# Kernel optimization log

Measured on AMD Instinct MI355X. Metric: run time of the kernel, lower is better.

Reference implementation:

```python
import jax, jax.numpy as jnp
import numpy as np

N, E, F, H, EF, ED, L, NL, NH, OD = 2048, 65536, 128, 512, 16, 64, 5, 4, 8, 64
MAX_DEG = 64


def _ln(x, s, b):
    m = x.mean(-1, keepdims=True)
    v = x.var(-1, keepdims=True)
    return (x - m) * jax.lax.rsqrt(v + 1e-5) * s + b


def setup_inputs() -> dict:
    key = jax.random.key(0)
    ks = jax.random.split(key, 40)
    s = 0.02
    x = jax.random.normal(ks[0], (N, F), jnp.float32)
    edge_index = jax.random.randint(ks[1], (2, E), 0, N, jnp.int32)
    edge_attr = jax.random.normal(ks[2], (E, EF), jnp.float32)
    # variable-length shortest paths, padded with -1
    plen = jax.random.randint(ks[3], (N, N), 0, L + 1, jnp.int32)
    pos = jnp.arange(L, dtype=jnp.int32)
    valid = pos[None, None, :] < plen[:, :, None]
    node_paths = jnp.where(valid, jax.random.randint(ks[4], (N, N, L), 0, N, jnp.int32), -1)
    edge_paths = jnp.where(valid, jax.random.randint(ks[5], (N, N, L), 0, E, jnp.int32), -1)
    p = {
        'x': x, 'edge_index': edge_index, 'edge_attr': edge_attr,
        'node_paths': node_paths, 'edge_paths': edge_paths,
        'W_node': s * jax.random.normal(ks[6], (F, H)), 'b_node': jnp.zeros((H,)),
        'W_edge': s * jax.random.normal(ks[7], (EF, ED)), 'b_edge': jnp.zeros((ED,)),
        'z_in': s * jax.random.normal(ks[8], (MAX_DEG, H)),
        'z_out': s * jax.random.normal(ks[9], (MAX_DEG, H)),
        'b_spatial': s * jax.random.normal(ks[10], (L,)),
        'edge_vector': s * jax.random.normal(ks[11], (L, ED)),
        'ln1_s': jnp.ones((NL, H)), 'ln1_b': jnp.zeros((NL, H)),
        'Wq': s * jax.random.normal(ks[12], (NL, H, H)), 'bq': jnp.zeros((NL, H)),
        'Wk': s * jax.random.normal(ks[13], (NL, H, H)), 'bk': jnp.zeros((NL, H)),
        'Wv': s * jax.random.normal(ks[14], (NL, H, H)), 'bv': jnp.zeros((NL, H)),
        'Wo': s * jax.random.normal(ks[15], (NL, H, H)), 'bo': jnp.zeros((NL, H)),
        'ln2_s': jnp.ones((NL, H)), 'ln2_b': jnp.zeros((NL, H)),
        'W1': s * jax.random.normal(ks[16], (NL, H, H)), 'b1': jnp.zeros((NL, H)),
        'W2': s * jax.random.normal(ks[17], (NL, H, H)), 'b2': jnp.zeros((NL, H)),
        'W_out': s * jax.random.normal(ks[18], (H, OD)), 'b_out': jnp.zeros((OD,)),
    }
    return p


def reference(x, edge_index, edge_attr, node_paths, edge_paths,
              W_node, b_node, W_edge, b_edge, z_in, z_out, b_spatial, edge_vector,
              ln1_s, ln1_b, Wq, bq, Wk, bk, Wv, bv, Wo, bo,
              ln2_s, ln2_b, W1, b1, W2, b2, W_out, b_out):
    n = x.shape[0]
    dk = H // NH
    h = x @ W_node + b_node  # [N,H]
    # centrality encoding: in/out degree -> learned embeddings, clamped
    in_deg = jnp.clip(jnp.zeros((n,), jnp.int32).at[edge_index[1]].add(1), 0, MAX_DEG - 1)
    out_deg = jnp.clip(jnp.zeros((n,), jnp.int32).at[edge_index[0]].add(1), 0, MAX_DEG - 1)
    h = h + z_in[in_deg] + z_out[out_deg]
    # edge encoding: mean over path of <edge_vector[k], edge_emb[path_k]>
    e_emb = edge_attr @ W_edge + b_edge           # [E,ED]
    w = e_emb @ edge_vector.T                     # [E,L] per-position dot products
    valid_e = edge_paths >= 0
    gath = w[jnp.clip(edge_paths, 0), jnp.arange(L)[None, None, :]]  # [N,N,L]
    cnt = valid_e.sum(-1).astype(h.dtype)
    c = jnp.where(cnt > 0, (gath * valid_e).sum(-1) / jnp.maximum(cnt, 1.0), 0.0)  # [N,N]
    # spatial encoding: learned scalar per path length
    plen = (node_paths >= 0).sum(-1)
    b_sp = jnp.where(plen > 0, b_spatial[jnp.clip(plen - 1, 0, L - 1)], 0.0)  # [N,N]
    bias = b_sp + c
    scale = 1.0 / jnp.sqrt(jnp.asarray(dk, h.dtype))
    for l in range(NL):
        y = _ln(h, ln1_s[l], ln1_b[l])
        q = (y @ Wq[l] + bq[l]).reshape(n, NH, dk)
        k = (y @ Wk[l] + bk[l]).reshape(n, NH, dk)
        v = (y @ Wv[l] + bv[l]).reshape(n, NH, dk)
        scores = jnp.einsum('ihd,jhd->hij', q, k) * scale + bias[None]
        attn = jax.nn.softmax(scores, axis=-1)
        o = jnp.einsum('hij,jhd->ihd', attn, v).reshape(n, H)
        h = h + o @ Wo[l] + bo[l]
        y2 = _ln(h, ln2_s[l], ln2_b[l])
        h = h + jax.nn.gelu(y2 @ W1[l] + b1[l]) @ W2[l] + b2[l]
    return h @ W_out + b_out
```

## Files before the change

### kernel.cpp

```cpp
#include <hip/hip_runtime.h>
#include <hip/hip_bf16.h>
#include <math.h>

#define N_NODES 2048
#define NEDGE   65536
#define FDIM    128
#define HDIM    512
#define EFD     16
#define EDD     64
#define LPATH   5
#define NLAYER  4
#define NHEAD   8
#define DK      64
#define ODIM    64
#define MAXDEG  64
#define PTOT    4194304

typedef __bf16 bf16;
typedef bf16 bf16x8 __attribute__((ext_vector_type(8)));
typedef bf16 bf16x4 __attribute__((ext_vector_type(4)));
typedef float f32x4 __attribute__((ext_vector_type(4)));
typedef unsigned short u16;

__global__ __launch_bounds__(256) void k_edge_w(const float* __restrict__ ea, const float* __restrict__ We,
                                                const float* __restrict__ be, const float* __restrict__ ev,
                                                const int* __restrict__ ei, int* __restrict__ din,
                                                int* __restrict__ dout, bf16* __restrict__ wT) {
    __shared__ float sM[80];
    __shared__ float sc[8];
    int t = threadIdx.x;
    if (t < 80) {
        int i = t / 5, j = t % 5;
        float acc = 0.f;
        for (int k = 0; k < EDD; ++k) acc += We[i * EDD + k] * ev[j * EDD + k];
        sM[t] = acc;
    } else if (t >= 128 && t < 128 + LPATH) {
        int j = t - 128;
        float acc = 0.f;
        for (int k = 0; k < EDD; ++k) acc += be[k] * ev[j * EDD + k];
        sc[j] = acc;
    }
    int e = blockIdx.x * 256 + t;
    atomicAdd(&dout[ei[e]], 1);
    atomicAdd(&din[ei[NEDGE + e]], 1);
    __syncthreads();
    const float4* p = (const float4*)(ea + (size_t)e * EFD);
    float4 a0 = p[0], a1 = p[1], a2 = p[2], a3 = p[3];
    float a[16] = {a0.x, a0.y, a0.z, a0.w, a1.x, a1.y, a1.z, a1.w,
                   a2.x, a2.y, a2.z, a2.w, a3.x, a3.y, a3.z, a3.w};
    float out[LPATH];
#pragma unroll
    for (int j = 0; j < LPATH; ++j) out[j] = sc[j];
#pragma unroll
    for (int i = 0; i < 16; ++i)
#pragma unroll
        for (int j = 0; j < LPATH; ++j) out[j] += a[i] * sM[i * LPATH + j];
#pragma unroll
    for (int j = 0; j < LPATH; ++j) wT[(size_t)j * NEDGE + e] = (bf16)out[j];
}

__global__ __launch_bounds__(1024) void k_bias3(const int* __restrict__ ep, const bf16* __restrict__ wT,
                                                const float* __restrict__ bsp, bf16* __restrict__ bias) {
    __shared__ char lds[163840];
    int t = threadIdx.x;
    size_t basep = (size_t)blockIdx.x * 8192;
    int* ish = (int*)lds;
    const int4* src = (const int4*)(ep + basep * 5);
#pragma unroll
    for (int u = 0; u < 10; ++u) ((int4*)ish)[t + 1024 * u] = src[t + 1024 * u];
    __syncthreads();
    unsigned pa[8], pb[8], pc[8];
#pragma unroll
    for (int r = 0; r < 8; ++r) {
        int p5 = (r * 1024 + t) * 5;
        int e0 = ish[p5], e1 = ish[p5 + 1], e2 = ish[p5 + 2], e3 = ish[p5 + 3], e4 = ish[p5 + 4];
        unsigned mk = (unsigned)(e0 >= 0) | ((unsigned)(e1 >= 0) << 1) | ((unsigned)(e2 >= 0) << 2)
                    | ((unsigned)(e3 >= 0) << 3) | ((unsigned)(e4 >= 0) << 4);
        pa[r] = ((unsigned)e0 & 0xFFFFu) | ((unsigned)e1 << 16);
        pb[r] = ((unsigned)e2 & 0xFFFFu) | ((unsigned)e3 << 16);
        pc[r] = ((unsigned)e4 & 0xFFFFu) | (mk << 16);
    }
    bf16* wsl = (bf16*)lds;
    float csum[8] = {};
#pragma unroll
    for (int l = 0; l < LPATH; ++l) {
        __syncthreads();
#pragma unroll
        for (int u = 0; u < 4; ++u) {
            int o = u * 16384 + t * 16;
            *(bf16x8*)&wsl[o]     = *(const bf16x8*)&wT[(size_t)l * NEDGE + o];
            *(bf16x8*)&wsl[o + 8] = *(const bf16x8*)&wT[(size_t)l * NEDGE + o + 8];
        }
        __syncthreads();
#pragma unroll
        for (int r = 0; r < 8; ++r) {
            unsigned ix = (l == 0) ? (pa[r] & 0xFFFFu) : (l == 1) ? (pa[r] >> 16)
                        : (l == 2) ? (pb[r] & 0xFFFFu) : (l == 3) ? (pb[r] >> 16) : (pc[r] & 0xFFFFu);
            float v = (float)wsl[ix];
            csum[r] += ((pc[r] >> (16 + l)) & 1u) ? v : 0.f;
        }
    }
#pragma unroll
    for (int r = 0; r < 8; ++r) {
        int cnt = __popc((int)((pc[r] >> 16) & 0x1Fu));
        float b = cnt ? bsp[cnt - 1] + csum[r] / (float)cnt : 0.f;
        bias[basep + r * 1024 + t] = (bf16)b;
    }
}

__global__ __launch_bounds__(256) void k_ln(const float* __restrict__ h, const float* __restrict__ sc,
                                            const float* __restrict__ bi, bf16* __restrict__ y) {
    int i = blockIdx.x, t = threadIdx.x;
    float v0 = h[(size_t)i * HDIM + t];
    float v1 = h[(size_t)i * HDIM + 256 + t];
    float s = v0 + v1, q = v0 * v0 + v1 * v1;
#pragma unroll
    for (int m = 1; m < 64; m <<= 1) { s += __shfl_xor(s, m); q += __shfl_xor(q, m); }
    __shared__ float ssum[4], sq[4];
    int wv = t >> 6;
    if ((t & 63) == 0) { ssum[wv] = s; sq[wv] = q; }
    __syncthreads();
    float S = ssum[0] + ssum[1] + ssum[2] + ssum[3];
    float Q = sq[0] + sq[1] + sq[2] + sq[3];
    float mean = S * (1.f / HDIM);
    float var = Q * (1.f / HDIM) - mean * mean;
    float r = rsqrtf(var + 1e-5f);
    y[(size_t)i * HDIM + t] = (bf16)((v0 - mean) * r * sc[t] + bi[t]);
    y[(size_t)i * HDIM + 256 + t] = (bf16)((v1 - mean) * r * sc[256 + t] + bi[256 + t]);
}

__global__ __launch_bounds__(256) void k_wprep(const float* __restrict__ Wq, const float* __restrict__ Wk,
                                               const float* __restrict__ Wv, const float* __restrict__ Wo,
                                               const float* __restrict__ W1, const float* __restrict__ W2,
                                               const float* __restrict__ Wn, bf16* __restrict__ Wt,
                                               bf16* __restrict__ WnT) {
    __shared__ float Ls[64][68];
    int m = blockIdx.y;
    int q = blockIdx.x;
    int t = threadIdx.x;
    int rr = t >> 4, cc = t & 15;
    int nl = t >> 2, kc = t & 3;
    if (m < 24) {
        int lay = m / 6, type = m % 6;
        const float* src = type == 0 ? Wq : type == 1 ? Wk : type == 2 ? Wv : type == 3 ? Wo : type == 4 ? W1 : W2;
        src += (size_t)lay * (HDIM * HDIM);
        int tk = q >> 3, tn = q & 7;
#pragma unroll
        for (int u = 0; u < 4; ++u) {
            float4 v = *(const float4*)(src + (size_t)(tk * 64 + rr + 16 * u) * HDIM + tn * 64 + cc * 4);
            *(float4*)&Ls[rr + 16 * u][cc * 4] = v;
        }
        __syncthreads();
        bf16 tmp[16];
#pragma unroll
        for (int u = 0; u < 16; ++u) tmp[u] = (bf16)Ls[kc * 16 + u][nl];
        bf16* dst = Wt + (size_t)m * (HDIM * HDIM) + (size_t)(tn * 64 + nl) * HDIM + tk * 64 + kc * 16;
        *(bf16x8*)(dst) = *(bf16x8*)&tmp[0];
        *(bf16x8*)(dst + 8) = *(bf16x8*)&tmp[8];
    } else {
        if (q >= 16) return;
        int tk = q >> 3, tn = q & 7;
#pragma unroll
        for (int u = 0; u < 4; ++u) {
            float4 v = *(const float4*)(Wn + (size_t)(tk * 64 + rr + 16 * u) * HDIM + tn * 64 + cc * 4);
            *(float4*)&Ls[rr + 16 * u][cc * 4] = v;
        }
        __syncthreads();
        bf16 tmp[16];
#pragma unroll
        for (int u = 0; u < 16; ++u) tmp[u] = (bf16)Ls[kc * 16 + u][nl];
        bf16* dst = WnT + (size_t)(tn * 64 + nl) * FDIM + tk * 64 + kc * 16;
        *(bf16x8*)dst = *(bf16x8*)&tmp[0];
        *(bf16x8*)(dst + 8) = *(bf16x8*)&tmp[8];
    }
}

__global__ __launch_bounds__(256) void k_nmm(const float* __restrict__ x, const bf16* __restrict__ Bt,
                                             const float* __restrict__ bn, const float* __restrict__ zin,
                                             const float* __restrict__ zout, const int* __restrict__ din,
                                             const int* __restrict__ dout, float* __restrict__ h) {
    __shared__ bf16 Bs[8192];
    int t = threadIdx.x, w = t >> 6, l = t & 63, lr = l & 15, lg = l >> 4;
    int j0 = blockIdx.x * 64, i0 = blockIdx.y * 64;
    const bf16* Bp = Bt + (size_t)j0 * FDIM;
#pragma unroll
    for (int rnd = 0; rnd < 4; ++rnd) {
        int tt = rnd * 256 + t;
        int ks = tt >> 8, qq = (tt >> 6) & 3, mm = (tt >> 2) & 15, gg = tt & 3;
        *(bf16x8*)(Bs + tt * 8) = *(const bf16x8*)(Bp + (size_t)(qq * 16 + mm) * FDIM + ks * 32 + gg * 8);
    }
    __syncthreads();
    const float* ap = x + (size_t)(i0 + w * 16 + lr) * FDIM + 8 * lg;
    f32x4 acc[4] = {};
#pragma unroll
    for (int ks = 0; ks < 4; ++ks) {
        float4 f0 = *(const float4*)(ap + ks * 32);
        float4 f1 = *(const float4*)(ap + ks * 32 + 4);
        bf16x8 a;
        a[0] = (bf16)f0.x; a[1] = (bf16)f0.y; a[2] = (bf16)f0.z; a[3] = (bf16)f0.w;
        a[4] = (bf16)f1.x; a[5] = (bf16)f1.y; a[6] = (bf16)f1.z; a[7] = (bf16)f1.w;
        const bf16* bb = Bs + ks * 2048 + lr * 32 + lg * 8;
#pragma unroll
        for (int sub = 0; sub < 4; ++sub)
            acc[sub] = __builtin_amdgcn_mfma_f32_16x16x32_bf16(a, *(const bf16x8*)(bb + sub * 512), acc[sub], 0, 0, 0);
    }
#pragma unroll
    for (int r = 0; r < 4; ++r) {
        int i = i0 + w * 16 + lg * 4 + r;
        int di = min(din[i], MAXDEG - 1), dz = min(dout[i], MAXDEG - 1);
#pragma unroll
        for (int sub = 0; sub < 4; ++sub) {
            int j = j0 + sub * 16 + lr;
            h[(size_t)i * HDIM + j] = acc[sub][r] + bn[j] + zin[(size_t)di * HDIM + j] + zout[(size_t)dz * HDIM + j];
        }
    }
}

__global__ __launch_bounds__(256) void k_qkv(const bf16* __restrict__ A, const bf16* __restrict__ Wt_l,
                                             const float* __restrict__ bq, const float* __restrict__ bk,
                                             const float* __restrict__ bv, bf16* __restrict__ qf,
                                             bf16* __restrict__ kf, bf16* __restrict__ vf) {
    __shared__ bf16 Bs[16384];
    int t = threadIdx.x, w = t >> 6, l = t & 63, lr = l & 15, lg = l >> 4;
    int j0 = blockIdx.x * 32, i0 = blockIdx.y * 64;
    int type = j0 >> 9, n0 = j0 & 511;
    const bf16* Bp = Wt_l + (size_t)type * (HDIM * HDIM) + (size_t)n0 * HDIM;
#pragma unroll
    for (int rnd = 0; rnd < 8; ++rnd) {
        int tt = rnd * 256 + t;
        int ks = tt >> 7, qq = (tt >> 6) & 1, mm = (tt >> 2) & 15, gg = tt & 3;
        bf16x8 v = *(const bf16x8*)(Bp + (size_t)(qq * 16 + mm) * HDIM + ks * 32 + gg * 8);
        *(bf16x8*)(Bs + tt * 8) = v;
    }
    __syncthreads();
    const bf16* ap = A + (size_t)(i0 + w * 16 + lr) * HDIM + 8 * lg;
    const float* bvec = (type == 0 ? bq : type == 1 ? bk : bv);
    f32x4 acc[2] = {};
#pragma unroll 4
    for (int ks = 0; ks < 16; ++ks) {
        bf16x8 a  = *(const bf16x8*)(ap + ks * 32);
        const bf16* bb = Bs + ks * 1024 + lr * 32 + lg * 8;
        bf16x8 b0 = *(const bf16x8*)(bb);
        bf16x8 b1 = *(const bf16x8*)(bb + 512);
        acc[0] = __builtin_amdgcn_mfma_f32_16x16x32_bf16(a, b0, acc[0], 0, 0, 0);
        acc[1] = __builtin_amdgcn_mfma_f32_16x16x32_bf16(a, b1, acc[1], 0, 0, 0);
    }
    int h = n0 >> 6;
    if (type < 2) {
        bf16* dst = (type == 0 ? qf : kf);
        int hf = (n0 & 32) >> 5;
        float sc = (type == 0 ? 0.125f : 1.0f);
#pragma unroll
        for (int sub = 0; sub < 2; ++sub) {
#pragma unroll
            for (int r = 0; r < 4; ++r) {
                int i = i0 + w * 16 + lg * 4 + r;
                float v = (acc[sub][r] + bvec[n0 + sub * 16 + lr]) * sc;
                int lgp = sub * 2 + (lr >> 3);
                size_t off = (((size_t)(h * 128 + (i >> 4)) * 2 + hf) << 9) + lgp * 128 + (lg * 4 + r) * 8 + (lr & 7);
                dst[off] = (bf16)v;
            }
        }
    } else {
#pragma unroll
        for (int sub = 0; sub < 2; ++sub) {
#pragma unroll
            for (int r = 0; r < 4; ++r) {
                int node = i0 + w * 16 + lg * 4 + r;
                int dd = (n0 & 63) + sub * 16 + lr;
                float v = acc[sub][r] + bvec[n0 + sub * 16 + lr];
                size_t off = (((size_t)(h * 4 + (dd >> 4)) * 64 + (node >> 5)) << 9)
                           + ((node >> 3) & 3) * 128 + (dd & 15) * 8 + (node & 7);
                vf[off] = (bf16)v;
            }
        }
    }
}

#define FL_RES   1
#define FL_GELU  2
#define FL_OUTF  4

__device__ inline float gelu_f(float x) {
    float x3 = x * x * x;
    float u = 0.7978845608028654f * (x + 0.044715f * x3);
    return 0.5f * x * (1.f + tanhf(u));
}

__global__ __launch_bounds__(1024) void k_mm(const bf16* __restrict__ A, const bf16* __restrict__ Bt,
                                             const float* __restrict__ bvec, const float* __restrict__ res,
                                             float* __restrict__ outF, bf16* __restrict__ outB, int flags) {
    __shared__ bf16 Bs[32768];
    __shared__ float Osh[4][16][68];
    int t = threadIdx.x, w = t >> 6, l = t & 63, lr = l & 15, lg = l >> 4;
    int ti = w & 3, s = w >> 2;
    int j0 = blockIdx.x * 64, i0 = blockIdx.y * 64;
    const bf16* Bp = Bt + (size_t)j0 * HDIM;
#pragma unroll
    for (int rnd = 0; rnd < 4; ++rnd) {
        int tt = rnd * 1024 + t;
        int ks = tt >> 8, qq = (tt >> 6) & 3, mm = (tt >> 2) & 15, gg = tt & 3;
        bf16x8 v = *(const bf16x8*)(Bp + (size_t)(qq * 16 + mm) * HDIM + ks * 32 + gg * 8);
        *(bf16x8*)(Bs + tt * 8) = v;
    }
    __syncthreads();
    const bf16* ap = A + (size_t)(i0 + ti * 16 + lr) * HDIM + 8 * lg;
    f32x4 acc[4] = {};
#pragma unroll
    for (int kk = 0; kk < 4; ++kk) {
        int ks = s * 4 + kk;
        bf16x8 a = *(const bf16x8*)(ap + ks * 32);
        const bf16* bb = Bs + ks * 2048 + lr * 32 + lg * 8;
#pragma unroll
        for (int sub = 0; sub < 4; ++sub) {
            bf16x8 b = *(const bf16x8*)(bb + sub * 512);
            acc[sub] = __builtin_amdgcn_mfma_f32_16x16x32_bf16(a, b, acc[sub], 0, 0, 0);
        }
    }
    if (s == 0) {
#pragma unroll
        for (int sub = 0; sub < 4; ++sub)
#pragma unroll
            for (int r = 0; r < 4; ++r) Osh[ti][lg * 4 + r][sub * 16 + lr] = acc[sub][r];
    }
    __syncthreads();
    if (s == 1) {
#pragma unroll
        for (int sub = 0; sub < 4; ++sub)
#pragma unroll
            for (int r = 0; r < 4; ++r) Osh[ti][lg * 4 + r][sub * 16 + lr] += acc[sub][r];
    }
    __syncthreads();
    if (s == 2) {
#pragma unroll
        for (int sub = 0; sub < 4; ++sub)
#pragma unroll
            for (int r = 0; r < 4; ++r) Osh[ti][lg * 4 + r][sub * 16 + lr] += acc[sub][r];
    }
    __syncthreads();
    if (s == 3) {
#pragma unroll
        for (int sub = 0; sub < 4; ++sub) {
#pragma unroll
            for (int r = 0; r < 4; ++r) {
                int i = i0 + ti * 16 + lg * 4 + r;
                int j = j0 + sub * 16 + lr;
                float v = Osh[ti][lg * 4 + r][sub * 16 + lr] + acc[sub][r] + bvec[j];
                if (flags & FL_RES) v += res[(size_t)i * HDIM + j];
                if (flags & FL_GELU) v = gelu_f(v);
                if (flags & FL_OUTF) outF[(size_t)i * HDIM + j] = v;
                else outB[(size_t)i * HDIM + j] = (bf16)v;
            }
        }
    }
}

__global__ __launch_bounds__(1024) void k_mmln(const float* __restrict__ h, const bf16* __restrict__ Bt,
                                               const float* __restrict__ lnS, const float* __restrict__ lnB,
                                               const float* __restrict__ bvec, bf16* __restrict__ outB) {
    __shared__ bf16 As[32768];
    __shared__ bf16 Bs[32768];
    __shared__ float Osh[4][16][68];
    __shared__ float sbuf[HDIM], bbuf[HDIM];
    int t = threadIdx.x, w = t >> 6, l = t & 63, lr = l & 15, lg = l >> 4;
    int ti = w & 3, s = w >> 2;
    int j0 = blockIdx.x * 64, i0 = blockIdx.y * 64;
    if (t < HDIM) sbuf[t] = lnS[t];
    else bbuf[t - HDIM] = lnB[t - HDIM];
    const bf16* Bp = Bt + (size_t)j0 * HDIM;
#pragma unroll
    for (int rnd = 0; rnd < 4; ++rnd) {
        int tt = rnd * 1024 + t;
        int ks = tt >> 8, qq = (tt >> 6) & 3, mm = (tt >> 2) & 15, gg = tt & 3;
        *(bf16x8*)(Bs + tt * 8) = *(const bf16x8*)(Bp + (size_t)(qq * 16 + mm) * HDIM + ks * 32 + gg * 8);
    }
    int row = t >> 4, ksc = t & 15;
    const float* hp = h + (size_t)(i0 + row) * HDIM + ksc * 32;
    float4 hv[8];
    float S = 0.f, Q = 0.f;
#pragma unroll
    for (int u = 0; u < 8; ++u) {
        hv[u] = *(const float4*)(hp + u * 4);
        S += hv[u].x + hv[u].y + hv[u].z + hv[u].w;
        Q += hv[u].x * hv[u].x + hv[u].y * hv[u].y + hv[u].z * hv[u].z + hv[u].w * hv[u].w;
    }
#pragma unroll
    for (int m = 1; m < 16; m <<= 1) { S += __shfl_xor(S, m); Q += __shfl_xor(Q, m); }
    float mean = S * (1.f / HDIM);
    float var = Q * (1.f / HDIM) - mean * mean;
    float rr = rsqrtf(var + 1e-5f);
    float ca = rr, cc = -mean * rr;
    __syncthreads();
    {
        bf16 tmp[32];
#pragma unroll
        for (int u = 0; u < 8; ++u) {
            float vv[4] = {hv[u].x, hv[u].y, hv[u].z, hv[u].w};
#pragma unroll
            for (int c = 0; c < 4; ++c) {
                int col = ksc * 32 + u * 4 + c;
                tmp[u * 4 + c] = (bf16)(fmaf(fmaf(vv[c], ca, cc), sbuf[col], bbuf[col]));
            }
        }
        bf16* dst = As + (row >> 4) * 8192 + ksc * 512 + (row & 15) * 32;
#pragma unroll
        for (int u = 0; u < 4; ++u) *(bf16x8*)(dst + u * 8) = *(bf16x8*)&tmp[u * 8];
    }
    __syncthreads();
    const bf16* apl = As + ti * 8192 + lr * 32 + lg * 8;
    f32x4 acc[4] = {};
#pragma unroll
    for (int kk = 0; kk < 4; ++kk) {
        int ks = s * 4 + kk;
        bf16x8 a = *(const bf16x8*)(apl + ks * 512);
        const bf16* bb = Bs + ks * 2048 + lr * 32 + lg * 8;
#pragma unroll
        for (int sub = 0; sub < 4; ++sub)
            acc[sub] = __builtin_amdgcn_mfma_f32_16x16x32_bf16(a, *(const bf16x8*)(bb + sub * 512), acc[sub], 0, 0, 0);
    }
    if (s == 0) {
#pragma unroll
        for (int sub = 0; sub < 4; ++sub)
#pragma unroll
            for (int r = 0; r < 4; ++r) Osh[ti][lg * 4 + r][sub * 16 + lr] = acc[sub][r];
    }
    __syncthreads();
    if (s == 1) {
#pragma unroll
        for (int sub = 0; sub < 4; ++sub)
#pragma unroll
            for (int r = 0; r < 4; ++r) Osh[ti][lg * 4 + r][sub * 16 + lr] += acc[sub][r];
    }
    __syncthreads();
    if (s == 2) {
#pragma unroll
        for (int sub = 0; sub < 4; ++sub)
#pragma unroll
            for (int r = 0; r < 4; ++r) Osh[ti][lg * 4 + r][sub * 16 + lr] += acc[sub][r];
    }
    __syncthreads();
    if (s == 3) {
#pragma unroll
        for (int sub = 0; sub < 4; ++sub) {
#pragma unroll
            for (int r = 0; r < 4; ++r) {
                int i = i0 + ti * 16 + lg * 4 + r;
                int j = j0 + sub * 16 + lr;
                float v = gelu_f(Osh[ti][lg * 4 + r][sub * 16 + lr] + acc[sub][r] + bvec[j]);
                outB[(size_t)i * HDIM + j] = (bf16)v;
            }
        }
    }
}

__global__ __launch_bounds__(1024) void k_attn2(const bf16* __restrict__ qf, const bf16* __restrict__ kf,
                                                const bf16* __restrict__ vf, const bf16* __restrict__ biasb,
                                                bf16* __restrict__ ob) {
    __shared__ char Pb[16 * 1024];
    __shared__ float Osh[4][64][17];
    __shared__ float Msh[4][4][16], Lsh[4][4][16];
    int t = threadIdx.x, w = t >> 6, l = t & 63, lr = l & 15, lg = l >> 4;
    int ti = w & 3, s = w >> 2;
    int bid = blockIdx.x;
    int wid = (bid & 7) * 32 + (bid >> 3);
    int i0 = (wid >> 3) * 64, hh = wid & 7;
    int irow = i0 + ti * 16;

    const bf16* qb = qf + (((size_t)(hh * 128 + (irow >> 4)) * 2) << 9) + l * 8;
    bf16x8 qy0 = *(const bf16x8*)(qb);
    bf16x8 qy1 = *(const bf16x8*)(qb + 512);

    char* pwr = Pb + w * 1024 + lr * 64;
    unsigned kx = (unsigned)(lr & 6) << 3;

    float m_run = -3e38f, l_run = 0.f;
    f32x4 oacc[4] = {};

    int jb0 = s * 512;
    const bf16* kbp = kf + (((size_t)(hh * 128 + (jb0 >> 4)) * 2) << 9) + l * 8;
    bf16x8 ka0 = *(const bf16x8*)(kbp);
    bf16x8 ka1 = *(const bf16x8*)(kbp + 512);
    bf16x8 ka2 = *(const bf16x8*)(kbp + 1024);
    bf16x8 ka3 = *(const bf16x8*)(kbp + 1536);
    const bf16* bpp = biasb + (size_t)(irow + lr) * N_NODES + jb0 + lg * 4;
    bf16x4 ba0 = *(const bf16x4*)(bpp);
    bf16x4 ba1 = *(const bf16x4*)(bpp + 16);

    for (int it = 0; it < 16; ++it) {
        int jb = s * 512 + it * 32;
        const bf16* vb = vf + (((size_t)(hh * 4) * 64 + (jb >> 5)) << 9) + l * 8;
        bf16x8 vx0 = *(const bf16x8*)(vb);
        bf16x8 vx1 = *(const bf16x8*)(vb + 32768);
        bf16x8 vx2 = *(const bf16x8*)(vb + 65536);
        bf16x8 vx3 = *(const bf16x8*)(vb + 98304);
        bf16x8 kn0, kn1, kn2, kn3;
        bf16x4 bn0, bn1;
        if (it < 15) {
            int jn = jb + 32;
            const bf16* kbn = kf + (((size_t)(hh * 128 + (jn >> 4)) * 2) << 9) + l * 8;
            kn0 = *(const bf16x8*)(kbn);
            kn1 = *(const bf16x8*)(kbn + 512);
            kn2 = *(const bf16x8*)(kbn + 1024);
            kn3 = *(const bf16x8*)(kbn + 1536);
            const bf16* bpn = biasb + (size_t)(irow + lr) * N_NODES + jn + lg * 4;
            bn0 = *(const bf16x4*)(bpn);
            bn1 = *(const bf16x4*)(bpn + 16);
        }

        f32x4 s0v = {}, s1v = {};
        __builtin_amdgcn_s_setprio(1);
        s0v = __builtin_amdgcn_mfma_f32_16x16x32_bf16(ka0, qy0, s0v, 0, 0, 0);
        s0v = __builtin_amdgcn_mfma_f32_16x16x32_bf16(ka1, qy1, s0v, 0, 0, 0);
        s1v = __builtin_amdgcn_mfma_f32_16x16x32_bf16(ka2, qy0, s1v, 0, 0, 0);
        s1v = __builtin_amdgcn_mfma_f32_16x16x32_bf16(ka3, qy1, s1v, 0, 0, 0);
        __builtin_amdgcn_s_setprio(0);

        float p0[4], p1[4];
        float mt = -3e38f;
#pragma unroll
        for (int r = 0; r < 4; ++r) {
            p0[r] = s0v[r] + (float)ba0[r];
            p1[r] = s1v[r] + (float)ba1[r];
            mt = fmaxf(mt, fmaxf(p0[r], p1[r]));
        }
        mt = fmaxf(mt, __shfl_xor(mt, 16));
        mt = fmaxf(mt, __shfl_xor(mt, 32));
        if (!__all(mt <= m_run + 8.f)) {
            float mn = fmaxf(m_run, mt);
            float alpha = __expf(m_run - mn);
            l_run *= alpha;
#pragma unroll
            for (int d = 0; d < 4; ++d) oacc[d] *= alpha;
            m_run = mn;
        }
        float ps = 0.f;
        bf16x4 pk0, pk1;
#pragma unroll
        for (int r = 0; r < 4; ++r) {
            p0[r] = __expf(p0[r] - m_run);
            p1[r] = __expf(p1[r] - m_run);
            ps += p0[r] + p1[r];
            pk0[r] = (bf16)p0[r];
            pk1[r] = (bf16)p1[r];
        }
        ps += __shfl_xor(ps, 16);
        ps += __shfl_xor(ps, 32);
        l_run += ps;

        *(bf16x4*)(pwr + ((lg * 8) ^ kx)) = pk0;
        *(bf16x4*)(pwr + ((32 + lg * 8) ^ kx)) = pk1;
        asm volatile("s_waitcnt lgkmcnt(0)" ::: "memory");
        __builtin_amdgcn_sched_barrier(0x20);
        bf16x8 py = *(bf16x8*)(Pb + w * 1024 + lr * 64 + ((lg * 16) ^ kx));
        __builtin_amdgcn_s_setprio(1);
        oacc[0] = __builtin_amdgcn_mfma_f32_16x16x32_bf16(vx0, py, oacc[0], 0, 0, 0);
        oacc[1] = __builtin_amdgcn_mfma_f32_16x16x32_bf16(vx1, py, oacc[1], 0, 0, 0);
        oacc[2] = __builtin_amdgcn_mfma_f32_16x16x32_bf16(vx2, py, oacc[2], 0, 0, 0);
        oacc[3] = __builtin_amdgcn_mfma_f32_16x16x32_bf16(vx3, py, oacc[3], 0, 0, 0);
        __builtin_amdgcn_s_setprio(0);
        ka0 = kn0; ka1 = kn1; ka2 = kn2; ka3 = kn3;
        ba0 = bn0; ba1 = bn1;
    }

    __syncthreads();
    if (lg == 0) { Msh[ti][s][lr] = m_run; Lsh[ti][s][lr] = l_run; }
    __syncthreads();
    float m0 = Msh[ti][0][lr], m1 = Msh[ti][1][lr], m2 = Msh[ti][2][lr], m3 = Msh[ti][3][lr];
    float mtot = fmaxf(fmaxf(m0, m1), fmaxf(m2, m3));
    float l_tot = Lsh[ti][0][lr] * __expf(m0 - mtot) + Lsh[ti][1][lr] * __expf(m1 - mtot)
                + Lsh[ti][2][lr] * __expf(m2 - mtot) + Lsh[ti][3][lr] * __expf(m3 - mtot);
    float fac = __expf(m_run - mtot);
#pragma unroll
    for (int d = 0; d < 4; ++d) oacc[d] *= fac;
    if (s == 0) {
#pragma unroll
        for (int db = 0; db < 4; ++db)
#pragma unroll
            for (int r = 0; r < 4; ++r) Osh[ti][db * 16 + lg * 4 + r][lr] = oacc[db][r];
    }
    __syncthreads();
    if (s == 1) {
#pragma unroll
        for (int db = 0; db < 4; ++db)
#pragma unroll
            for (int r = 0; r < 4; ++r) Osh[ti][db * 16 + lg * 4 + r][lr] += oacc[db][r];
    }
    __syncthreads();
    if (s == 2) {
#pragma unroll
        for (int db = 0; db < 4; ++db)
#pragma unroll
            for (int r = 0; r < 4; ++r) Osh[ti][db * 16 + lg * 4 + r][lr] += oacc[db][r];
    }
    __syncthreads();
    if (s == 3) {
        float inv = 1.f / l_tot;
#pragma unroll
        for (int db = 0; db < 4; ++db) {
            bf16x4 o4;
#pragma unroll
            for (int r = 0; r < 4; ++r)
                o4[r] = (bf16)((Osh[ti][db * 16 + lg * 4 + r][lr] + oacc[db][r]) * inv);
            *(bf16x4*)(ob + (size_t)(irow + lr) * HDIM + hh * DK + db * 16 + lg * 4) = o4;
        }
    }
}

__global__ __launch_bounds__(256) void k_gemm(const float* __restrict__ A, const float* __restrict__ B,
                                              const float* __restrict__ bvec, float* __restrict__ C,
                                              int M, int Nc, int K) {
    __shared__ float As[16][68];
    __shared__ float Bs[16][68];
    int t = threadIdx.x;
    int tm = t >> 4, tn = t & 15;
    int i0 = blockIdx.y * 64, j0 = blockIdx.x * 64;
    int ar = t >> 2, aq = t & 3;
    int br = t >> 4, bq = t & 15;
    float acc[4][4] = {};
    for (int k0 = 0; k0 < K; k0 += 16) {
        float4 av = *(const float4*)(A + (size_t)(i0 + ar) * K + k0 + aq * 4);
        As[aq * 4 + 0][ar] = av.x;
        As[aq * 4 + 1][ar] = av.y;
        As[aq * 4 + 2][ar] = av.z;
        As[aq * 4 + 3][ar] = av.w;
        *(float4*)&Bs[br][bq * 4] = *(const float4*)(B + (size_t)(k0 + br) * Nc + j0 + bq * 4);
        __syncthreads();
#pragma unroll
        for (int k = 0; k < 16; ++k) {
            float4 a4 = *(const float4*)&As[k][tm * 4];
            float4 b4 = *(const float4*)&Bs[k][tn * 4];
            float avv[4] = {a4.x, a4.y, a4.z, a4.w};
            float bvv[4] = {b4.x, b4.y, b4.z, b4.w};
#pragma unroll
            for (int r = 0; r < 4; ++r)
#pragma unroll
                for (int c = 0; c < 4; ++c) acc[r][c] += avv[r] * bvv[c];
        }
        __syncthreads();
    }
#pragma unroll
    for (int r = 0; r < 4; ++r) {
#pragma unroll
        for (int c = 0; c < 4; ++c) {
            int i = i0 + tm * 4 + r;
            int j = j0 + tn * 4 + c;
            C[(size_t)i * Nc + j] = acc[r][c] + bvec[j];
        }
    }
}

extern "C" void kernel_launch(void* const* d_in, const int* in_sizes, int n_in,
                              void* d_out, int out_size, void* d_ws, size_t ws_size,
                              hipStream_t stream) {
    const float* x      = (const float*)d_in[0];
    const int*   ei     = (const int*)d_in[1];
    const float* eattr  = (const float*)d_in[2];
    const int*   epaths = (const int*)d_in[4];
    const float* Wn     = (const float*)d_in[5];
    const float* bn     = (const float*)d_in[6];
    const float* We     = (const float*)d_in[7];
    const float* be     = (const float*)d_in[8];
    const float* zin    = (const float*)d_in[9];
    const float* zout   = (const float*)d_in[10];
    const float* bsp    = (const float*)d_in[11];
    const float* ev     = (const float*)d_in[12];
    const float* ln1s   = (const float*)d_in[13];
    const float* ln1b   = (const float*)d_in[14];
    const float* Wq     = (const float*)d_in[15];
    const float* bq     = (const float*)d_in[16];
    const float* Wk     = (const float*)d_in[17];
    const float* bk     = (const float*)d_in[18];
    const float* Wv     = (const float*)d_in[19];
    const float* bv     = (const float*)d_in[20];
    const float* Wo     = (const float*)d_in[21];
    const float* bo     = (const float*)d_in[22];
    const float* ln2s   = (const float*)d_in[23];
    const float* ln2b   = (const float*)d_in[24];
    const float* W1     = (const float*)d_in[25];
    const float* b1     = (const float*)d_in[26];
    const float* W2     = (const float*)d_in[27];
    const float* b2     = (const float*)d_in[28];
    const float* Wout   = (const float*)d_in[29];
    const float* bout   = (const float*)d_in[30];

    char* base = (char*)d_ws;
    size_t off = 0;
    auto alloc = [&](size_t bytes) { char* p = base + off; off = (off + bytes + 255) & ~(size_t)255; return p; };
    bf16*  bias   = (bf16*)alloc((size_t)N_NODES * N_NODES * 2);
    float* h      = (float*)alloc((size_t)N_NODES * HDIM * 4);
    bf16*  wT     = (bf16*)alloc((size_t)LPATH * NEDGE * 2);
    int*   deg    = (int*)alloc(2 * N_NODES * 4);
    bf16*  WnT    = (bf16*)alloc((size_t)HDIM * FDIM * 2);
    bf16*  Wt     = (bf16*)alloc((size_t)NLAYER * 6 * HDIM * HDIM * 2);
    bf16*  y_bf   = (bf16*)alloc((size_t)N_NODES * HDIM * 2);
    bf16*  qfb    = (bf16*)alloc((size_t)NHEAD * 128 * 2 * 512 * 2);
    bf16*  kfb    = (bf16*)alloc((size_t)NHEAD * 128 * 2 * 512 * 2);
    bf16*  vfb    = (bf16*)alloc((size_t)NHEAD * 4 * 64 * 512 * 2);
    bf16*  ob_bf  = (bf16*)alloc((size_t)N_NODES * HDIM * 2);
    bf16*  t1_bf  = (bf16*)alloc((size_t)N_NODES * HDIM * 2);
    int* din = deg;
    int* dout = deg + N_NODES;

    hipMemsetAsync(deg, 0, 2 * N_NODES * sizeof(int), stream);

    k_edge_w<<<NEDGE / 256, 256, 0, stream>>>(eattr, We, be, ev, ei, din, dout, wT);
    k_bias3<<<512, 1024, 0, stream>>>(epaths, wT, bsp, bias);
    k_wprep<<<dim3(64, 25), 256, 0, stream>>>(Wq, Wk, Wv, Wo, W1, W2, Wn, Wt, WnT);
    k_nmm<<<dim3(8, 32), 256, 0, stream>>>(x, WnT, bn, zin, zout, din, dout, h);

    dim3 gqkv(48, 32);
    dim3 gmm(8, 32);

    for (int lay = 0; lay < NLAYER; ++lay) {
        const bf16* Wt_l = Wt + (size_t)lay * 6 * HDIM * HDIM;
        size_t bOff = (size_t)lay * HDIM;
        k_ln<<<N_NODES, 256, 0, stream>>>(h, ln1s + bOff, ln1b + bOff, y_bf);
        k_qkv<<<gqkv, 256, 0, stream>>>(y_bf, Wt_l, bq + bOff, bk + bOff, bv + bOff, qfb, kfb, vfb);
        k_attn2<<<256, 1024, 0, stream>>>(qfb, kfb, vfb, bias, ob_bf);
        k_mm<<<gmm, 1024, 0, stream>>>(ob_bf, Wt_l + (size_t)3 * HDIM * HDIM, bo + bOff, h, h, nullptr, FL_RES | FL_OUTF);
        k_mmln<<<gmm, 1024, 0, stream>>>(h, Wt_l + (size_t)4 * HDIM * HDIM, ln2s + bOff, ln2b + bOff, b1 + bOff, t1_bf);
        k_mm<<<gmm, 1024, 0, stream>>>(t1_bf, Wt_l + (size_t)5 * HDIM * HDIM, b2 + bOff, h, h, nullptr, FL_RES | FL_OUTF);
    }
    k_gemm<<<dim3(1, 32), 256, 0, stream>>>(h, Wout, bout, (float*)d_out, N_NODES, ODIM, HDIM);
}
```

Baseline: 481.2 us.

## Double-buffer bias gather, warp-per-row layernorm, and MFMA output projection

```diff
diff --git a/kernel.cpp b/kernel.cpp
--- a/kernel.cpp
+++ b/kernel.cpp
@@ -64,6 +64,9 @@
     __shared__ char lds[163840];
     int t = threadIdx.x;
     size_t basep = (size_t)blockIdx.x * 8192;
+    bf16x8 pre[4];
+#pragma unroll
+    for (int u = 0; u < 4; ++u) pre[u] = *(const bf16x8*)(wT + u * 8192 + t * 8);
     int* ish = (int*)lds;
     const int4* src = (const int4*)(ep + basep * 5);
 #pragma unroll
@@ -80,25 +83,40 @@
         pb[r] = ((unsigned)e2 & 0xFFFFu) | ((unsigned)e3 << 16);
         pc[r] = ((unsigned)e4 & 0xFFFFu) | (mk << 16);
     }
-    bf16* wsl = (bf16*)lds;
+    __syncthreads();
+    {
+        bf16* b0 = (bf16*)lds;
+#pragma unroll
+        for (int u = 0; u < 4; ++u) *(bf16x8*)(b0 + u * 8192 + t * 8) = pre[u];
+    }
+    __syncthreads();
     float csum[8] = {};
-#pragma unroll
-    for (int l = 0; l < LPATH; ++l) {
-        __syncthreads();
-#pragma unroll
-        for (int u = 0; u < 4; ++u) {
-            int o = u * 16384 + t * 16;
-            *(bf16x8*)&wsl[o]     = *(const bf16x8*)&wT[(size_t)l * NEDGE + o];
-            *(bf16x8*)&wsl[o + 8] = *(const bf16x8*)&wT[(size_t)l * NEDGE + o + 8];
-        }
-        __syncthreads();
+    int cur = 0;
+#pragma unroll
+    for (int s = 0; s < 10; ++s) {
+        int l = s >> 1, half = s & 1;
+        bf16x8 nxt[4];
+        if (s < 9) {
+            const bf16* wn = wT + (size_t)((s + 1) >> 1) * NEDGE + ((s + 1) & 1) * 32768;
+#pragma unroll
+            for (int u = 0; u < 4; ++u) nxt[u] = *(const bf16x8*)(wn + u * 8192 + t * 8);
+        }
+        const bf16* bc = (const bf16*)lds + cur * 32768;
 #pragma unroll
         for (int r = 0; r < 8; ++r) {
             unsigned ix = (l == 0) ? (pa[r] & 0xFFFFu) : (l == 1) ? (pa[r] >> 16)
                         : (l == 2) ? (pb[r] & 0xFFFFu) : (l == 3) ? (pb[r] >> 16) : (pc[r] & 0xFFFFu);
-            float v = (float)wsl[ix];
-            csum[r] += ((pc[r] >> (16 + l)) & 1u) ? v : 0.f;
-        }
+            bool hit = (((pc[r] >> (16 + l)) & 1u) != 0) && ((ix >> 15) == (unsigned)half);
+            if (hit) csum[r] += (float)bc[ix & 32767u];
+        }
+        __syncthreads();
+        if (s < 9) {
+            bf16* ba = (bf16*)lds + (cur ^ 1) * 32768;
+#pragma unroll
+            for (int u = 0; u < 4; ++u) *(bf16x8*)(ba + u * 8192 + t * 8) = nxt[u];
+            cur ^= 1;
+        }
+        __syncthreads();
     }
 #pragma unroll
     for (int r = 0; r < 8; ++r) {
@@ -110,30 +128,36 @@
 
 __global__ __launch_bounds__(256) void k_ln(const float* __restrict__ h, const float* __restrict__ sc,
                                             const float* __restrict__ bi, bf16* __restrict__ y) {
-    int i = blockIdx.x, t = threadIdx.x;
-    float v0 = h[(size_t)i * HDIM + t];
-    float v1 = h[(size_t)i * HDIM + 256 + t];
-    float s = v0 + v1, q = v0 * v0 + v1 * v1;
+    int t = threadIdx.x, w = t >> 6, l = t & 63;
+    int row = blockIdx.x * 4 + w;
+    const float* hp = h + (size_t)row * HDIM + l * 8;
+    float4 a = *(const float4*)hp;
+    float4 b = *(const float4*)(hp + 4);
+    float s = a.x + a.y + a.z + a.w + b.x + b.y + b.z + b.w;
+    float q = a.x * a.x + a.y * a.y + a.z * a.z + a.w * a.w
+            + b.x * b.x + b.y * b.y + b.z * b.z + b.w * b.w;
 #pragma unroll
     for (int m = 1; m < 64; m <<= 1) { s += __shfl_xor(s, m); q += __shfl_xor(q, m); }
-    __shared__ float ssum[4], sq[4];
-    int wv = t >> 6;
-    if ((t & 63) == 0) { ssum[wv] = s; sq[wv] = q; }
-    __syncthreads();
-    float S = ssum[0] + ssum[1] + ssum[2] + ssum[3];
-    float Q = sq[0] + sq[1] + sq[2] + sq[3];
-    float mean = S * (1.f / HDIM);
-    float var = Q * (1.f / HDIM) - mean * mean;
+    float mean = s * (1.f / HDIM);
+    float var = q * (1.f / HDIM) - mean * mean;
     float r = rsqrtf(var + 1e-5f);
-    y[(size_t)i * HDIM + t] = (bf16)((v0 - mean) * r * sc[t] + bi[t]);
-    y[(size_t)i * HDIM + 256 + t] = (bf16)((v1 - mean) * r * sc[256 + t] + bi[256 + t]);
+    float4 s0 = *(const float4*)(sc + l * 8), s1 = *(const float4*)(sc + l * 8 + 4);
+    float4 b0 = *(const float4*)(bi + l * 8), b1 = *(const float4*)(bi + l * 8 + 4);
+    float va[8] = {a.x, a.y, a.z, a.w, b.x, b.y, b.z, b.w};
+    float ss[8] = {s0.x, s0.y, s0.z, s0.w, s1.x, s1.y, s1.z, s1.w};
+    float bb[8] = {b0.x, b0.y, b0.z, b0.w, b1.x, b1.y, b1.z, b1.w};
+    bf16x8 o;
+#pragma unroll
+    for (int c = 0; c < 8; ++c) o[c] = (bf16)((va[c] - mean) * r * ss[c] + bb[c]);
+    *(bf16x8*)(y + (size_t)row * HDIM + l * 8) = o;
 }
 
 __global__ __launch_bounds__(256) void k_wprep(const float* __restrict__ Wq, const float* __restrict__ Wk,
                                                const float* __restrict__ Wv, const float* __restrict__ Wo,
                                                const float* __restrict__ W1, const float* __restrict__ W2,
-                                               const float* __restrict__ Wn, bf16* __restrict__ Wt,
-                                               bf16* __restrict__ WnT) {
+                                               const float* __restrict__ Wn, const float* __restrict__ Wout,
+                                               bf16* __restrict__ Wt, bf16* __restrict__ WnT,
+                                               bf16* __restrict__ WoutT) {
     __shared__ float Ls[64][68];
     int m = blockIdx.y;
     int q = blockIdx.x;
@@ -157,7 +181,7 @@
         bf16* dst = Wt + (size_t)m * (HDIM * HDIM) + (size_t)(tn * 64 + nl) * HDIM + tk * 64 + kc * 16;
         *(bf16x8*)(dst) = *(bf16x8*)&tmp[0];
         *(bf16x8*)(dst + 8) = *(bf16x8*)&tmp[8];
-    } else {
+    } else if (m == 24) {
         if (q >= 16) return;
         int tk = q >> 3, tn = q & 7;
 #pragma unroll
@@ -170,6 +194,21 @@
 #pragma unroll
         for (int u = 0; u < 16; ++u) tmp[u] = (bf16)Ls[kc * 16 + u][nl];
         bf16* dst = WnT + (size_t)(tn * 64 + nl) * FDIM + tk * 64 + kc * 16;
+        *(bf16x8*)dst = *(bf16x8*)&tmp[0];
+        *(bf16x8*)(dst + 8) = *(bf16x8*)&tmp[8];
+    } else {
+        if (q >= 8) return;
+        int tk = q;
+#pragma unroll
+        for (int u = 0; u < 4; ++u) {
+            float4 v = *(const float4*)(Wout + (size_t)(tk * 64 + rr + 16 * u) * ODIM + cc * 4);
+            *(float4*)&Ls[rr + 16 * u][cc * 4] = v;
+        }
+        __syncthreads();
+        bf16 tmp[16];
+#pragma unroll
+        for (int u = 0; u < 16; ++u) tmp[u] = (bf16)Ls[kc * 16 + u][nl];
+        bf16* dst = WoutT + (size_t)nl * HDIM + tk * 64 + kc * 16;
         *(bf16x8*)dst = *(bf16x8*)&tmp[0];
         *(bf16x8*)(dst + 8) = *(bf16x8*)&tmp[8];
     }
@@ -606,45 +645,56 @@
     }
 }
 
-__global__ __launch_bounds__(256) void k_gemm(const float* __restrict__ A, const float* __restrict__ B,
-                                              const float* __restrict__ bvec, float* __restrict__ C,
-                                              int M, int Nc, int K) {
-    __shared__ float As[16][68];
-    __shared__ float Bs[16][68];
-    int t = threadIdx.x;
-    int tm = t >> 4, tn = t & 15;
-    int i0 = blockIdx.y * 64, j0 = blockIdx.x * 64;
-    int ar = t >> 2, aq = t & 3;
-    int br = t >> 4, bq = t & 15;
-    float acc[4][4] = {};
-    for (int k0 = 0; k0 < K; k0 += 16) {
-        float4 av = *(const float4*)(A + (size_t)(i0 + ar) * K + k0 + aq * 4);
-        As[aq * 4 + 0][ar] = av.x;
-        As[aq * 4 + 1][ar] = av.y;
-        As[aq * 4 + 2][ar] = av.z;
-        As[aq * 4 + 3][ar] = av.w;
-        *(float4*)&Bs[br][bq * 4] = *(const float4*)(B + (size_t)(k0 + br) * Nc + j0 + bq * 4);
-        __syncthreads();
-#pragma unroll
-        for (int k = 0; k < 16; ++k) {
-            float4 a4 = *(const float4*)&As[k][tm * 4];
-            float4 b4 = *(const float4*)&Bs[k][tn * 4];
-            float avv[4] = {a4.x, a4.y, a4.z, a4.w};
-            float bvv[4] = {b4.x, b4.y, b4.z, b4.w};
-#pragma unroll
-            for (int r = 0; r < 4; ++r)
-#pragma unroll
-                for (int c = 0; c < 4; ++c) acc[r][c] += avv[r] * bvv[c];
-        }
-        __syncthreads();
-    }
-#pragma unroll
-    for (int r = 0; r < 4; ++r) {
-#pragma unroll
-        for (int c = 0; c < 4; ++c) {
-            int i = i0 + tm * 4 + r;
-            int j = j0 + tn * 4 + c;
-            C[(size_t)i * Nc + j] = acc[r][c] + bvec[j];
+__global__ __launch_bounds__(256) void k_fout(const float* __restrict__ h, const bf16* __restrict__ Bt,
+                                              const float* __restrict__ bvec, float* __restrict__ C) {
+    __shared__ float Osh[16][68];
+    int t = threadIdx.x, s = t >> 6, l = t & 63, lr = l & 15, lg = l >> 4;
+    int i0 = blockIdx.x * 16;
+    const float* ap = h + (size_t)(i0 + lr) * HDIM + s * 128 + lg * 8;
+    f32x4 acc[4] = {};
+#pragma unroll
+    for (int kk = 0; kk < 4; ++kk) {
+        float4 f0 = *(const float4*)(ap + kk * 32);
+        float4 f1 = *(const float4*)(ap + kk * 32 + 4);
+        bf16x8 a;
+        a[0] = (bf16)f0.x; a[1] = (bf16)f0.y; a[2] = (bf16)f0.z; a[3] = (bf16)f0.w;
+        a[4] = (bf16)f1.x; a[5] = (bf16)f1.y; a[6] = (bf16)f1.z; a[7] = (bf16)f1.w;
+#pragma unroll
+        for (int sub = 0; sub < 4; ++sub) {
+            bf16x8 b = *(const bf16x8*)(Bt + (size_t)(sub * 16 + lr) * HDIM + s * 128 + kk * 32 + lg * 8);
+            acc[sub] = __builtin_amdgcn_mfma_f32_16x16x32_bf16(a, b, acc[sub], 0, 0, 0);
+        }
+    }
+    if (s == 0) {
+#pragma unroll
+        for (int sub = 0; sub < 4; ++sub)
+#pragma unroll
+            for (int r = 0; r < 4; ++r) Osh[lg * 4 + r][sub * 16 + lr] = acc[sub][r];
+    }
+    __syncthreads();
+    if (s == 1) {
+#pragma unroll
+        for (int sub = 0; sub < 4; ++sub)
+#pragma unroll
+            for (int r = 0; r < 4; ++r) Osh[lg * 4 + r][sub * 16 + lr] += acc[sub][r];
+    }
+    __syncthreads();
+    if (s == 2) {
+#pragma unroll
+        for (int sub = 0; sub < 4; ++sub)
+#pragma unroll
+            for (int r = 0; r < 4; ++r) Osh[lg * 4 + r][sub * 16 + lr] += acc[sub][r];
+    }
+    __syncthreads();
+    if (s == 3) {
+#pragma unroll
+        for (int sub = 0; sub < 4; ++sub) {
+#pragma unroll
+            for (int r = 0; r < 4; ++r) {
+                int i = i0 + lg * 4 + r;
+                int j = sub * 16 + lr;
+                C[(size_t)i * ODIM + j] = Osh[lg * 4 + r][sub * 16 + lr] + acc[sub][r] + bvec[j];
+            }
         }
     }
 }
@@ -691,6 +741,7 @@
     bf16*  wT     = (bf16*)alloc((size_t)LPATH * NEDGE * 2);
     int*   deg    = (int*)alloc(2 * N_NODES * 4);
     bf16*  WnT    = (bf16*)alloc((size_t)HDIM * FDIM * 2);
+    bf16*  WoutT  = (bf16*)alloc((size_t)ODIM * HDIM * 2);
     bf16*  Wt     = (bf16*)alloc((size_t)NLAYER * 6 * HDIM * HDIM * 2);
     bf16*  y_bf   = (bf16*)alloc((size_t)N_NODES * HDIM * 2);
     bf16*  qfb    = (bf16*)alloc((size_t)NHEAD * 128 * 2 * 512 * 2);
@@ -705,7 +756,7 @@
 
     k_edge_w<<<NEDGE / 256, 256, 0, stream>>>(eattr, We, be, ev, ei, din, dout, wT);
     k_bias3<<<512, 1024, 0, stream>>>(epaths, wT, bsp, bias);
-    k_wprep<<<dim3(64, 25), 256, 0, stream>>>(Wq, Wk, Wv, Wo, W1, W2, Wn, Wt, WnT);
+    k_wprep<<<dim3(64, 26), 256, 0, stream>>>(Wq, Wk, Wv, Wo, W1, W2, Wn, Wout, Wt, WnT, WoutT);
     k_nmm<<<dim3(8, 32), 256, 0, stream>>>(x, WnT, bn, zin, zout, din, dout, h);
 
     dim3 gqkv(48, 32);
@@ -714,12 +765,12 @@
     for (int lay = 0; lay < NLAYER; ++lay) {
         const bf16* Wt_l = Wt + (size_t)lay * 6 * HDIM * HDIM;
         size_t bOff = (size_t)lay * HDIM;
-        k_ln<<<N_NODES, 256, 0, stream>>>(h, ln1s + bOff, ln1b + bOff, y_bf);
+        k_ln<<<512, 256, 0, stream>>>(h, ln1s + bOff, ln1b + bOff, y_bf);
         k_qkv<<<gqkv, 256, 0, stream>>>(y_bf, Wt_l, bq + bOff, bk + bOff, bv + bOff, qfb, kfb, vfb);
         k_attn2<<<256, 1024, 0, stream>>>(qfb, kfb, vfb, bias, ob_bf);
         k_mm<<<gmm, 1024, 0, stream>>>(ob_bf, Wt_l + (size_t)3 * HDIM * HDIM, bo + bOff, h, h, nullptr, FL_RES | FL_OUTF);
         k_mmln<<<gmm, 1024, 0, stream>>>(h, Wt_l + (size_t)4 * HDIM * HDIM, ln2s + bOff, ln2b + bOff, b1 + bOff, t1_bf);
         k_mm<<<gmm, 1024, 0, stream>>>(t1_bf, Wt_l + (size_t)5 * HDIM * HDIM, b2 + bOff, h, h, nullptr, FL_RES | FL_OUTF);
     }
-    k_gemm<<<dim3(1, 32), 256, 0, stream>>>(h, Wout, bout, (float*)d_out, N_NODES, ODIM, HDIM);
-}
+    k_fout<<<128, 256, 0, stream>>>(h, WoutT, bout, (float*)d_out);
+}
```

Measured after the change: 462.5 us. 1.04x faster.
